# Optimization experiments

Hardware: AMD Instinct MI355X
Metric: run time of the kernel (lower is better)

The kernel has to match this reference:

```python
import jax, jax.numpy as jnp
import numpy as np

EMB_DIM = 1024
D_K = 64
B, S = 4, 4096

def setup_inputs() -> dict:
    key = jax.random.key(0)
    ks = jax.random.split(key, 8)
    inv = 1.0 / np.sqrt(EMB_DIM)
    return {
        "input1": jax.random.normal(ks[0], (B, S, EMB_DIM), dtype=jnp.float32),
        "input2": jax.random.normal(ks[1], (B, S, EMB_DIM), dtype=jnp.float32),
        "Wq": jax.random.uniform(ks[2], (EMB_DIM, D_K), jnp.float32, -inv, inv),
        "bq": jax.random.uniform(ks[3], (D_K,), jnp.float32, -inv, inv),
        "Wk": jax.random.uniform(ks[4], (EMB_DIM, D_K), jnp.float32, -inv, inv),
        "bk": jax.random.uniform(ks[5], (D_K,), jnp.float32, -inv, inv),
        "Wv": jax.random.uniform(ks[6], (EMB_DIM, D_K), jnp.float32, -inv, inv),
        "bv": jax.random.uniform(ks[7], (D_K,), jnp.float32, -inv, inv),
    }

def reference(input1, input2, Wq, bq, Wk, bk, Wv, bv):
    # queries from input2; keys/values from input1 (as in the torch forward)
    q = input2 @ Wq + bq            # [B, Sq, d_k]
    k = input1 @ Wk + bk            # [B, Sk, d_k]
    v = input1 @ Wv + bv            # [B, Sk, d_k]
    scale = 1.0 / jnp.sqrt(jnp.asarray(D_K, q.dtype))
    scores = jnp.einsum("bqd,bkd->bqk", q, k) * scale  # [B, Sq, Sk]
    attn = jax.nn.softmax(scores, axis=-1)
    return jnp.einsum("bqk,bkd->bqd", attn, v)          # [B, Sq, d_k]
```

## Files before the change

kernel.cpp:

```cpp
#include <hip/hip_runtime.h>
#include <hip/hip_bf16.h>

#define E 1024
#define DK 64
#define SEQ 4096
#define NB 4
#define KSCALE 0.18033688011112042f

typedef short bf16x8 __attribute__((ext_vector_type(8)));
typedef short bf16x4 __attribute__((ext_vector_type(4)));
typedef float f32x4 __attribute__((ext_vector_type(4)));

typedef const __attribute__((address_space(1))) unsigned int* gcp;
typedef __attribute__((address_space(3))) unsigned int* lcp;

__device__ inline unsigned short f2bf(float f) {
    unsigned int u = __float_as_uint(f);
    u += 0x7fff + ((u >> 16) & 1);
    return (unsigned short)(u >> 16);
}
__device__ inline unsigned int cvtpk(float a, float b) {
    union { __hip_bfloat162 h; unsigned int u; } x;
    x.h = __float22bfloat162_rn(make_float2(a, b));
    return x.u;
}
__device__ inline bf16x8 cvt8(f32x4 a, f32x4 b) {
    union { unsigned int u[4]; bf16x8 v; } x;
    x.u[0] = cvtpk(a[0], a[1]); x.u[1] = cvtpk(a[2], a[3]);
    x.u[2] = cvtpk(b[0], b[1]); x.u[3] = cvtpk(b[2], b[3]);
    return x.v;
}

__global__ __launch_bounds__(256) void wt_kernel(
    const float* __restrict__ Wq, const float* __restrict__ Wk, const float* __restrict__ Wv,
    unsigned short* __restrict__ wtq, unsigned short* __restrict__ wtk, unsigned short* __restrict__ wtv)
{
    const float* src; unsigned short* dst;
    if (blockIdx.y == 0)      { src = Wq; dst = wtq; }
    else if (blockIdx.y == 1) { src = Wk; dst = wtk; }
    else                      { src = Wv; dst = wtv; }
    const int tid = threadIdx.x;
    const int e0 = blockIdx.x * 64;
    __shared__ float Ws[64][65];
    #pragma unroll
    for (int i = 0; i < 4; ++i) {
        int flat = i * 256 + tid;
        int r = flat >> 4;
        int c4 = (flat & 15) << 2;
        float4 v = *reinterpret_cast<const float4*>(&src[(size_t)(e0 + r) * DK + c4]);
        Ws[c4 + 0][r] = v.x; Ws[c4 + 1][r] = v.y; Ws[c4 + 2][r] = v.z; Ws[c4 + 3][r] = v.w;
    }
    __syncthreads();
    #pragma unroll
    for (int i = 0; i < 4; ++i) {
        int flat = i * 256 + tid;
        int c = flat >> 4;
        int r4 = (flat & 15) << 2;
        ushort4 o;
        o.x = f2bf(Ws[c][r4 + 0]); o.y = f2bf(Ws[c][r4 + 1]);
        o.z = f2bf(Ws[c][r4 + 2]); o.w = f2bf(Ws[c][r4 + 3]);
        *reinterpret_cast<ushort4*>(&dst[(size_t)c * E + e0 + r4]) = o;
    }
}

__global__ __launch_bounds__(256, 4) void proj_kernel(
    const float* __restrict__ in_q, const float* __restrict__ in_kv,
    const unsigned short* __restrict__ wtq, const unsigned short* __restrict__ wtk,
    const unsigned short* __restrict__ wtv,
    const float* __restrict__ bq, const float* __restrict__ bk, const float* __restrict__ bv,
    unsigned short* __restrict__ Qw, unsigned short* __restrict__ Kw, unsigned short* __restrict__ Vtw)
{
    const int tid = threadIdx.x;
    const int w = tid >> 6, lane = tid & 63, quad = lane >> 4, l16 = lane & 15;
    const int row0 = blockIdx.x * 64;
    const bool isQ = (blockIdx.y == 0);
    const float* Arow = (isQ ? in_q : in_kv) + (size_t)(row0 + w * 16 + l16) * E;
    const unsigned short* w0 = isQ ? wtq : wtk;

    __shared__ unsigned short W0s[2][4096];
    __shared__ unsigned short W1s[2][4096];

    const int rl = lane >> 3, pp = lane & 7;

    #pragma unroll
    for (int i = 0; i < 2; ++i) {
        int g = w * 2 + i;
        int r = g * 8 + rl;
        int lc = pp ^ (r & 7);
        __builtin_amdgcn_global_load_lds((gcp)(const void*)(w0 + (size_t)r * E + lc * 8),
                                         (lcp)(void*)&W0s[0][g * 512], 16, 0, 0);
        if (!isQ)
            __builtin_amdgcn_global_load_lds((gcp)(const void*)(wtv + (size_t)r * E + lc * 8),
                                             (lcp)(void*)&W1s[0][g * 512], 16, 0, 0);
    }
    f32x4 a_cur[4];
    #pragma unroll
    for (int ks = 0; ks < 2; ++ks)
        #pragma unroll
        for (int j = 0; j < 2; ++j)
            a_cur[ks * 2 + j] = *reinterpret_cast<const f32x4*>(Arow + ks * 32 + quad * 8 + j * 4);
    __syncthreads();

    f32x4 acc0[4] = {};
    f32x4 acc1[4] = {};

    for (int kb = 0; kb < 16; ++kb) {
        const int cur = kb & 1, nxt = cur ^ 1;
        f32x4 a_nxt[4];
        if (kb < 15) {
            const int ko = (kb + 1) * 64;
            #pragma unroll
            for (int i = 0; i < 2; ++i) {
                int g = w * 2 + i;
                int r = g * 8 + rl;
                int lc = pp ^ (r & 7);
                __builtin_amdgcn_global_load_lds((gcp)(const void*)(w0 + (size_t)r * E + ko + lc * 8),
                                                 (lcp)(void*)&W0s[nxt][g * 512], 16, 0, 0);
                if (!isQ)
                    __builtin_amdgcn_global_load_lds((gcp)(const void*)(wtv + (size_t)r * E + ko + lc * 8),
                                                     (lcp)(void*)&W1s[nxt][g * 512], 16, 0, 0);
            }
            const float* an = Arow + ko;
            #pragma unroll
            for (int ks = 0; ks < 2; ++ks)
                #pragma unroll
                for (int j = 0; j < 2; ++j)
                    a_nxt[ks * 2 + j] = *reinterpret_cast<const f32x4*>(an + ks * 32 + quad * 8 + j * 4);
        }
        #pragma unroll
        for (int ks = 0; ks < 2; ++ks) {
            bf16x8 af = cvt8(a_cur[ks * 2], a_cur[ks * 2 + 1]);
            #pragma unroll
            for (int ct = 0; ct < 4; ++ct) {
                int brow = ct * 16 + l16;
                int pc = (ks * 4 + quad) ^ (brow & 7);
                bf16x8 b0 = *reinterpret_cast<const bf16x8*>(&W0s[cur][brow * 64 + pc * 8]);
                acc0[ct] = __builtin_amdgcn_mfma_f32_16x16x32_bf16(af, b0, acc0[ct], 0, 0, 0);
                if (!isQ) {
                    bf16x8 b1 = *reinterpret_cast<const bf16x8*>(&W1s[cur][brow * 64 + pc * 8]);
                    acc1[ct] = __builtin_amdgcn_mfma_f32_16x16x32_bf16(af, b1, acc1[ct], 0, 0, 0);
                }
            }
        }
        #pragma unroll
        for (int j = 0; j < 4; ++j) a_cur[j] = a_nxt[j];
        if (kb < 15) __syncthreads();
    }

    const int orow0 = row0 + w * 16 + quad * 4;
    #pragma unroll
    for (int ct = 0; ct < 4; ++ct) {
        int col = ct * 16 + l16;
        if (isQ) {
            float bias = bq[col];
            #pragma unroll
            for (int r = 0; r < 4; ++r)
                Qw[(size_t)(orow0 + r) * DK + col] = f2bf(acc0[ct][r] + bias);
        } else {
            float biask = bk[col], biasv = bv[col];
            #pragma unroll
            for (int r = 0; r < 4; ++r) {
                int grow = orow0 + r;
                Kw[(size_t)grow * DK + col] = f2bf((acc0[ct][r] + biask) * KSCALE);
                int bb = grow >> 12;
                int tok = grow & 4095;
                Vtw[((size_t)(bb * 64 + col)) * SEQ + tok] = f2bf(acc1[ct][r] + biasv);
            }
        }
    }
}

__global__ __launch_bounds__(512) void attn_kernel(
    const unsigned short* __restrict__ Qw, const unsigned short* __restrict__ Kw,
    const unsigned short* __restrict__ Vtw, float* __restrict__ out)
{
    const int tid = threadIdx.x;
    const int w = tid >> 6, lane = tid & 63, quad = lane >> 4, l16 = lane & 15;
    const int wk = w & 3, wp = w >> 2;
    const int b = (blockIdx.x & 7) >> 1;
    const int qt = ((blockIdx.x >> 3) << 1) | (blockIdx.x & 1);

    __shared__ float LDSf[8][2][16][68];
    __shared__ float LDSl[8][4][16];

    bf16x8 qfb[2][4];
    #pragma unroll
    for (int ks = 0; ks < 2; ++ks)
        #pragma unroll
        for (int ct = 0; ct < 4; ++ct)
            qfb[ks][ct] = *reinterpret_cast<const bf16x8*>(
                &Qw[((size_t)(b * SEQ + qt * 64 + ct * 16 + l16)) * DK + ks * 32 + quad * 8]);

    const unsigned short* Kp = Kw + ((size_t)(b * SEQ) + wk * 16 + l16) * DK;
    const unsigned short* Vp[4];
    #pragma unroll
    for (int ct = 0; ct < 4; ++ct)
        Vp[ct] = Vtw + ((size_t)(b * 64 + ct * 16 + l16)) * SEQ + wk * 16 + quad * 4;

    bf16x8 kf_c0 = *reinterpret_cast<const bf16x8*>(Kp + (size_t)wp * 64 * DK + quad * 8);
    bf16x8 kf_c1 = *reinterpret_cast<const bf16x8*>(Kp + (size_t)wp * 64 * DK + 32 + quad * 8);
    bf16x4 va_c[4];
    #pragma unroll
    for (int ct = 0; ct < 4; ++ct)
        va_c[ct] = *reinterpret_cast<const bf16x4*>(Vp[ct] + (size_t)wp * 64);

    float lp[4] = {0.f, 0.f, 0.f, 0.f};
    f32x4 o[4][4] = {};

    #pragma unroll 1
    for (int i = 0; i < 32; ++i) {
        bf16x8 kf_n0, kf_n1;
        bf16x4 va_n[4];
        if (i < 31) {
            const size_t koff = (size_t)(2 * (i + 1) + wp) * 64;
            kf_n0 = *reinterpret_cast<const bf16x8*>(Kp + koff * DK + quad * 8);
            kf_n1 = *reinterpret_cast<const bf16x8*>(Kp + koff * DK + 32 + quad * 8);
            #pragma unroll
            for (int ct = 0; ct < 4; ++ct)
                va_n[ct] = *reinterpret_cast<const bf16x4*>(Vp[ct] + koff);
        }

        f32x4 sacc[4] = {};
        #pragma unroll
        for (int ct = 0; ct < 4; ++ct) {
            sacc[ct] = __builtin_amdgcn_mfma_f32_16x16x32_bf16(kf_c0, qfb[0][ct], sacc[ct], 0, 0, 0);
            sacc[ct] = __builtin_amdgcn_mfma_f32_16x16x32_bf16(kf_c1, qfb[1][ct], sacc[ct], 0, 0, 0);
        }

        #pragma unroll
        for (int cq = 0; cq < 4; ++cq) {
            float p0 = __builtin_amdgcn_exp2f(sacc[cq][0]);
            float p1 = __builtin_amdgcn_exp2f(sacc[cq][1]);
            float p2 = __builtin_amdgcn_exp2f(sacc[cq][2]);
            float p3 = __builtin_amdgcn_exp2f(sacc[cq][3]);
            lp[cq] += (p0 + p1) + (p2 + p3);
            union { unsigned int u[2]; bf16x4 v; } pbu;
            pbu.u[0] = cvtpk(p0, p1);
            pbu.u[1] = cvtpk(p2, p3);
            bf16x4 pb = pbu.v;
            #pragma unroll
            for (int cd = 0; cd < 4; ++cd)
                o[cd][cq] = __builtin_amdgcn_mfma_f32_16x16x16bf16_1k(va_c[cd], pb, o[cd][cq], 0, 0, 0);
        }

        kf_c0 = kf_n0; kf_c1 = kf_n1;
        #pragma unroll
        for (int ct = 0; ct < 4; ++ct) va_c[ct] = va_n[ct];
    }

    #pragma unroll
    for (int cq = 0; cq < 4; ++cq) {
        float t = lp[cq];
        t += __shfl_xor(t, 16, 64);
        t += __shfl_xor(t, 32, 64);
        lp[cq] = t;
    }
    if (lane < 16)
        #pragma unroll
        for (int cq = 0; cq < 4; ++cq)
            LDSl[w][cq][lane] = lp[cq];

    #pragma unroll
    for (int rr = 0; rr < 2; ++rr) {
        #pragma unroll
        for (int hh = 0; hh < 2; ++hh)
            #pragma unroll
            for (int cd = 0; cd < 4; ++cd)
                *reinterpret_cast<f32x4*>(&LDSf[w][hh][l16][cd * 16 + quad * 4]) = o[cd][rr * 2 + hh];
        __syncthreads();
        {
            const int hh = tid >> 8;
            const int cq = rr * 2 + hh;
            const int ql = (tid >> 4) & 15;
            const int d4 = (tid & 15) << 2;
            f32x4 acc = {};
            #pragma unroll
            for (int w2 = 0; w2 < 8; ++w2)
                acc += *reinterpret_cast<const f32x4*>(&LDSf[w2][hh][ql][d4]);
            float lq = 0.f;
            #pragma unroll
            for (int w2 = 0; w2 < 8; ++w2)
                lq += LDSl[w2][cq][ql];
            f32x4 res = acc * (1.0f / lq);
            *reinterpret_cast<f32x4*>(&out[((size_t)(b * SEQ + qt * 64 + cq * 16 + ql)) * DK + d4]) = res;
        }
        __syncthreads();
    }
}

extern "C" void kernel_launch(void* const* d_in, const int* in_sizes, int n_in,
                              void* d_out, int out_size, void* d_ws, size_t ws_size,
                              hipStream_t stream) {
    const float* input1 = (const float*)d_in[0];
    const float* input2 = (const float*)d_in[1];
    const float* Wq = (const float*)d_in[2];
    const float* bq = (const float*)d_in[3];
    const float* Wk = (const float*)d_in[4];
    const float* bk = (const float*)d_in[5];
    const float* Wv = (const float*)d_in[6];
    const float* bv = (const float*)d_in[7];
    float* out = (float*)d_out;

    char* ws = (char*)d_ws;
    unsigned short* wtq = (unsigned short*)(ws + 0);
    unsigned short* wtk = (unsigned short*)(ws + 131072);
    unsigned short* wtv = (unsigned short*)(ws + 262144);
    unsigned short* Qw  = (unsigned short*)(ws + 393216);
    unsigned short* Kw  = (unsigned short*)(ws + 2490368);
    unsigned short* Vtw = (unsigned short*)(ws + 4587520);

    wt_kernel<<<dim3(16, 3), 256, 0, stream>>>(Wq, Wk, Wv, wtq, wtk, wtv);
    proj_kernel<<<dim3(256, 2), 256, 0, stream>>>(input2, input1, wtq, wtk, wtv,
                                                  bq, bk, bv, Qw, Kw, Vtw);
    attn_kernel<<<dim3(256), 512, 0, stream>>>(Qw, Kw, Vtw, out);
}
```

Before: 213.6 us.

## Stage K/V tiles through double-buffered swizzled LDS via global_load_lds

Replaces the per-wave direct global register prefetch of K and V fragments with cooperative async global-to-LDS copies (global_load_lds) into double-buffered, XOR-swizzled shared tiles. Each iteration prefetches the next 128-key tile while computing on the current one, then reads fragments from LDS. The aim is to stop the 8 waves in a block from each fetching overlapping K/V data, and to make the global accesses coalesced. The cost is extra LDS usage, which may lower occupancy, and a block-wide barrier every iteration. The loop is also unrolled by 2.

```diff
diff --git a/kernel.cpp b/kernel.cpp
--- a/kernel.cpp
+++ b/kernel.cpp
@@ -180,8 +180,35 @@
     const int b = (blockIdx.x & 7) >> 1;
     const int qt = ((blockIdx.x >> 3) << 1) | (blockIdx.x & 1);
 
+    __shared__ unsigned short Klds[2][8192];
+    __shared__ unsigned short Vlds[2][8192];
     __shared__ float LDSf[8][2][16][68];
     __shared__ float LDSl[8][4][16];
+
+    const unsigned short* Ksrc = Kw + (size_t)b * SEQ * DK;
+    const unsigned short* Vsrc = Vtw + (size_t)b * 64 * SEQ;
+
+    const int g0 = w * 2, g1 = w * 2 + 1;
+    const int krow0 = g0 * 8 + (lane >> 3), krow1 = g1 * 8 + (lane >> 3);
+    const int kcol = ((lane & 7) ^ (lane >> 3)) << 4;
+    const int vrow0 = g0 * 4 + (lane >> 4), vrow1 = g1 * 4 + (lane >> 4);
+    const int vcol0 = ((lane & 15) ^ (vrow0 & 7)) << 4;
+    const int vcol1 = ((lane & 15) ^ (vrow1 & 7)) << 4;
+
+    auto stage = [&](int t, int bb) {
+        const char* kb = (const char*)Ksrc + (size_t)t * 16384;
+        __builtin_amdgcn_global_load_lds((gcp)(const void*)(kb + krow0 * 128 + kcol),
+                                         (lcp)(void*)((char*)Klds[bb] + g0 * 1024), 16, 0, 0);
+        __builtin_amdgcn_global_load_lds((gcp)(const void*)(kb + krow1 * 128 + kcol),
+                                         (lcp)(void*)((char*)Klds[bb] + g1 * 1024), 16, 0, 0);
+        const char* vb = (const char*)Vsrc + t * 256;
+        __builtin_amdgcn_global_load_lds((gcp)(const void*)(vb + (size_t)vrow0 * 8192 + vcol0),
+                                         (lcp)(void*)((char*)Vlds[bb] + g0 * 1024), 16, 0, 0);
+        __builtin_amdgcn_global_load_lds((gcp)(const void*)(vb + (size_t)vrow1 * 8192 + vcol1),
+                                         (lcp)(void*)((char*)Vlds[bb] + g1 * 1024), 16, 0, 0);
+    };
+
+    stage(0, 0);
 
     bf16x8 qfb[2][4];
     #pragma unroll
@@ -191,40 +218,38 @@
             qfb[ks][ct] = *reinterpret_cast<const bf16x8*>(
                 &Qw[((size_t)(b * SEQ + qt * 64 + ct * 16 + l16)) * DK + ks * 32 + quad * 8]);
 
-    const unsigned short* Kp = Kw + ((size_t)(b * SEQ) + wk * 16 + l16) * DK;
-    const unsigned short* Vp[4];
+    const int kxor = (l16 & 7) << 4;
+    const int krow = wp * 64 + wk * 16 + l16;
+    const unsigned kf0_off = (unsigned)(krow * 128 + ((quad * 16) ^ kxor));
+    const unsigned kf1_off = (unsigned)(krow * 128 + ((64 + quad * 16) ^ kxor));
+    unsigned va_off[4];
     #pragma unroll
     for (int ct = 0; ct < 4; ++ct)
-        Vp[ct] = Vtw + ((size_t)(b * 64 + ct * 16 + l16)) * SEQ + wk * 16 + quad * 4;
-
-    bf16x8 kf_c0 = *reinterpret_cast<const bf16x8*>(Kp + (size_t)wp * 64 * DK + quad * 8);
-    bf16x8 kf_c1 = *reinterpret_cast<const bf16x8*>(Kp + (size_t)wp * 64 * DK + 32 + quad * 8);
-    bf16x4 va_c[4];
-    #pragma unroll
-    for (int ct = 0; ct < 4; ++ct)
-        va_c[ct] = *reinterpret_cast<const bf16x4*>(Vp[ct] + (size_t)wp * 64);
+        va_off[ct] = (unsigned)((ct * 16 + l16) * 256 +
+                                ((wp * 128 + wk * 32 + quad * 8) ^ kxor));
+
+    __syncthreads();
 
     float lp[4] = {0.f, 0.f, 0.f, 0.f};
     f32x4 o[4][4] = {};
 
-    #pragma unroll 1
+    #pragma unroll 2
     for (int i = 0; i < 32; ++i) {
-        bf16x8 kf_n0, kf_n1;
-        bf16x4 va_n[4];
-        if (i < 31) {
-            const size_t koff = (size_t)(2 * (i + 1) + wp) * 64;
-            kf_n0 = *reinterpret_cast<const bf16x8*>(Kp + koff * DK + quad * 8);
-            kf_n1 = *reinterpret_cast<const bf16x8*>(Kp + koff * DK + 32 + quad * 8);
-            #pragma unroll
-            for (int ct = 0; ct < 4; ++ct)
-                va_n[ct] = *reinterpret_cast<const bf16x4*>(Vp[ct] + koff);
-        }
+        const int cur = i & 1;
+        if (i < 31) stage(i + 1, cur ^ 1);
+
+        bf16x8 kf0 = *reinterpret_cast<const bf16x8*>((const char*)Klds[cur] + kf0_off);
+        bf16x8 kf1 = *reinterpret_cast<const bf16x8*>((const char*)Klds[cur] + kf1_off);
+        bf16x4 va[4];
+        #pragma unroll
+        for (int ct = 0; ct < 4; ++ct)
+            va[ct] = *reinterpret_cast<const bf16x4*>((const char*)Vlds[cur] + va_off[ct]);
 
         f32x4 sacc[4] = {};
         #pragma unroll
         for (int ct = 0; ct < 4; ++ct) {
-            sacc[ct] = __builtin_amdgcn_mfma_f32_16x16x32_bf16(kf_c0, qfb[0][ct], sacc[ct], 0, 0, 0);
-            sacc[ct] = __builtin_amdgcn_mfma_f32_16x16x32_bf16(kf_c1, qfb[1][ct], sacc[ct], 0, 0, 0);
+            sacc[ct] = __builtin_amdgcn_mfma_f32_16x16x32_bf16(kf0, qfb[0][ct], sacc[ct], 0, 0, 0);
+            sacc[ct] = __builtin_amdgcn_mfma_f32_16x16x32_bf16(kf1, qfb[1][ct], sacc[ct], 0, 0, 0);
         }
 
         #pragma unroll
@@ -240,12 +265,10 @@
             bf16x4 pb = pbu.v;
             #pragma unroll
             for (int cd = 0; cd < 4; ++cd)
-                o[cd][cq] = __builtin_amdgcn_mfma_f32_16x16x16bf16_1k(va_c[cd], pb, o[cd][cq], 0, 0, 0);
-        }
-
-        kf_c0 = kf_n0; kf_c1 = kf_n1;
-        #pragma unroll
-        for (int ct = 0; ct < 4; ++ct) va_c[ct] = va_n[ct];
+                o[cd][cq] = __builtin_amdgcn_mfma_f32_16x16x16bf16_1k(va[cd], pb, o[cd][cq], 0, 0, 0);
+        }
+
+        __syncthreads();
     }
 
     #pragma unroll
```

Result: no change. 209.6 us (-1.9%).

## Stage projection outputs in LDS for coalesced stores; split attention keys across 16 warps

Applied to the files above, without the earlier changes.

The projection kernel now writes Q/K and the transposed V tiles into shared memory first, then stores them to global memory as 16-byte vectors. This replaces the scattered 2-byte stores, especially the strided transposed V writes. The attention kernel doubles its block to 1024 threads (16 warps), so each warp handles half as many key chunks, and the LDS reduction covers 16 partial sums. The larger block raises per-block LDS use and register pressure under launch bounds of 1024, and the final reduction becomes longer.

```diff
diff --git a/kernel.cpp b/kernel.cpp
--- a/kernel.cpp
+++ b/kernel.cpp
@@ -10,6 +10,7 @@
 typedef short bf16x8 __attribute__((ext_vector_type(8)));
 typedef short bf16x4 __attribute__((ext_vector_type(4)));
 typedef float f32x4 __attribute__((ext_vector_type(4)));
+typedef unsigned short u16x8 __attribute__((ext_vector_type(8)));
 
 typedef const __attribute__((address_space(1))) unsigned int* gcp;
 typedef __attribute__((address_space(3))) unsigned int* lcp;
@@ -79,6 +80,8 @@
 
     __shared__ unsigned short W0s[2][4096];
     __shared__ unsigned short W1s[2][4096];
+    __shared__ unsigned short Cs0[64][68];
+    __shared__ unsigned short Cs1[64][68];
 
     const int rl = lane >> 3, pp = lane & 7;
 
@@ -147,7 +150,7 @@
         if (kb < 15) __syncthreads();
     }
 
-    const int orow0 = row0 + w * 16 + quad * 4;
+    const int tl0 = w * 16 + quad * 4;
     #pragma unroll
     for (int ct = 0; ct < 4; ++ct) {
         int col = ct * 16 + l16;
@@ -155,22 +158,35 @@
             float bias = bq[col];
             #pragma unroll
             for (int r = 0; r < 4; ++r)
-                Qw[(size_t)(orow0 + r) * DK + col] = f2bf(acc0[ct][r] + bias);
+                Cs0[tl0 + r][col] = f2bf(acc0[ct][r] + bias);
         } else {
             float biask = bk[col], biasv = bv[col];
             #pragma unroll
             for (int r = 0; r < 4; ++r) {
-                int grow = orow0 + r;
-                Kw[(size_t)grow * DK + col] = f2bf((acc0[ct][r] + biask) * KSCALE);
-                int bb = grow >> 12;
-                int tok = grow & 4095;
-                Vtw[((size_t)(bb * 64 + col)) * SEQ + tok] = f2bf(acc1[ct][r] + biasv);
+                Cs0[tl0 + r][col] = f2bf((acc0[ct][r] + biask) * KSCALE);
+                Cs1[col][tl0 + r] = f2bf(acc1[ct][r] + biasv);
             }
         }
     }
-}
-
-__global__ __launch_bounds__(512) void attn_kernel(
+    __syncthreads();
+
+    const int bb = row0 >> 12, tok0 = row0 & 4095;
+    #pragma unroll
+    for (int jj = 0; jj < 2; ++jj) {
+        int rr = w * 16 + jj * 8 + (lane >> 3);
+        int c8 = (lane & 7) * 8;
+        u16x8 v0 = *reinterpret_cast<const u16x8*>(&Cs0[rr][c8]);
+        if (isQ) {
+            *reinterpret_cast<u16x8*>(&Qw[(size_t)(row0 + rr) * DK + c8]) = v0;
+        } else {
+            *reinterpret_cast<u16x8*>(&Kw[(size_t)(row0 + rr) * DK + c8]) = v0;
+            u16x8 v1 = *reinterpret_cast<const u16x8*>(&Cs1[rr][c8]);
+            *reinterpret_cast<u16x8*>(&Vtw[((size_t)(bb * 64 + rr)) * SEQ + tok0 + c8]) = v1;
+        }
+    }
+}
+
+__global__ __launch_bounds__(1024) void attn_kernel(
     const unsigned short* __restrict__ Qw, const unsigned short* __restrict__ Kw,
     const unsigned short* __restrict__ Vtw, float* __restrict__ out)
 {
@@ -180,8 +196,8 @@
     const int b = (blockIdx.x & 7) >> 1;
     const int qt = ((blockIdx.x >> 3) << 1) | (blockIdx.x & 1);
 
-    __shared__ float LDSf[8][2][16][68];
-    __shared__ float LDSl[8][4][16];
+    __shared__ float LDSf[16][2][16][68];
+    __shared__ float LDSl[16][4][16];
 
     bf16x8 qfb[2][4];
     #pragma unroll
@@ -208,11 +224,11 @@
     f32x4 o[4][4] = {};
 
     #pragma unroll 1
-    for (int i = 0; i < 32; ++i) {
+    for (int i = 0; i < 16; ++i) {
         bf16x8 kf_n0, kf_n1;
         bf16x4 va_n[4];
-        if (i < 31) {
-            const size_t koff = (size_t)(2 * (i + 1) + wp) * 64;
+        if (i < 15) {
+            const size_t koff = (size_t)(4 * (i + 1) + wp) * 64;
             kf_n0 = *reinterpret_cast<const bf16x8*>(Kp + koff * DK + quad * 8);
             kf_n1 = *reinterpret_cast<const bf16x8*>(Kp + koff * DK + 32 + quad * 8);
             #pragma unroll
@@ -268,18 +284,18 @@
             for (int cd = 0; cd < 4; ++cd)
                 *reinterpret_cast<f32x4*>(&LDSf[w][hh][l16][cd * 16 + quad * 4]) = o[cd][rr * 2 + hh];
         __syncthreads();
-        {
+        if (tid < 512) {
             const int hh = tid >> 8;
             const int cq = rr * 2 + hh;
             const int ql = (tid >> 4) & 15;
             const int d4 = (tid & 15) << 2;
             f32x4 acc = {};
             #pragma unroll
-            for (int w2 = 0; w2 < 8; ++w2)
+            for (int w2 = 0; w2 < 16; ++w2)
                 acc += *reinterpret_cast<const f32x4*>(&LDSf[w2][hh][ql][d4]);
             float lq = 0.f;
             #pragma unroll
-            for (int w2 = 0; w2 < 8; ++w2)
+            for (int w2 = 0; w2 < 16; ++w2)
                 lq += LDSl[w2][cq][ql];
             f32x4 res = acc * (1.0f / lq);
             *reinterpret_cast<f32x4*>(&out[((size_t)(b * SEQ + qt * 64 + cq * 16 + ql)) * DK + d4]) = res;
@@ -312,5 +328,5 @@
     wt_kernel<<<dim3(16, 3), 256, 0, stream>>>(Wq, Wk, Wv, wtq, wtk, wtv);
     proj_kernel<<<dim3(256, 2), 256, 0, stream>>>(input2, input1, wtq, wtk, wtv,
                                                   bq, bk, bv, Qw, Kw, Vtw);
-    attn_kernel<<<dim3(256), 512, 0, stream>>>(Qw, Kw, Vtw, out);
-}
+    attn_kernel<<<dim3(256), 1024, 0, stream>>>(Qw, Kw, Vtw, out);
+}
```

Result: slower. 265.2 us (+24.1%).
